# Kernel tuning notes

Hardware: AMD Instinct MI355X
Metric: run time of the kernel (lower is better)

## Reference

```python
import jax, jax.numpy as jnp
import numpy as np

N, E, IN, H, C = 50000, 800000, 128, 256, 2
EPS = 1e-5


def setup_inputs() -> dict:
    key = jax.random.key(0)
    ks = jax.random.split(key, 12)
    inp = {
        "x": jax.random.normal(ks[0], (N, IN), jnp.float32),
        "edge_index": jax.random.randint(ks[1], (2, E), 0, N, jnp.int32),
        "w_nei0": jax.random.normal(ks[2], (IN, H), jnp.float32) * 0.05,
        "w_root0": jax.random.normal(ks[3], (IN, H), jnp.float32) * 0.05,
        "b0": jnp.zeros((H,), jnp.float32),
        "w_nei": jax.random.normal(ks[4], (2, H, H), jnp.float32) * 0.05,
        "w_root": jax.random.normal(ks[5], (2, H, H), jnp.float32) * 0.05,
        "b": jnp.zeros((2, H), jnp.float32),
        "bn_gamma": jnp.ones((3, H), jnp.float32),
        "bn_beta": jnp.zeros((3, H), jnp.float32),
        "bn_mean": jax.random.normal(ks[6], (3, H), jnp.float32) * 0.05,
        "bn_var": jnp.ones((3, H), jnp.float32),
        "w1": jax.random.normal(ks[7], (H, H // 2), jnp.float32) * 0.05,
        "b1": jnp.zeros((H // 2,), jnp.float32),
        "w2": jax.random.normal(ks[8], (H // 2, C), jnp.float32) * 0.05,
        "b2": jnp.zeros((C,), jnp.float32),
    }
    return inp


def _mean_aggregate(h, src, dst, inv_deg):
    # gather source-node features, scatter-sum to destinations, divide by degree
    agg = jax.ops.segment_sum(h[src], dst, num_segments=N)  # (N, d)
    return agg * inv_deg[:, None]


def _forward(x, edge_index, w_nei0, w_root0, b0, w_nei, w_root, b,
             bn_gamma, bn_beta, bn_mean, bn_var, w1, b1, w2, b2):
    src, dst = edge_index[0], edge_index[1]
    deg = jax.ops.segment_sum(jnp.ones((E,), x.dtype), dst, num_segments=N)
    inv_deg = 1.0 / jnp.maximum(deg, 1.0)

    h = x
    wn_list = [w_nei0, w_nei[0], w_nei[1]]
    wr_list = [w_root0, w_root[0], w_root[1]]
    bias_list = [b0, b[0], b[1]]
    for i in range(3):
        mean_nb = _mean_aggregate(h, src, dst, inv_deg)          # (N, d_in)
        h = mean_nb @ wn_list[i] + bias_list[i] + h @ wr_list[i]  # SAGEConv
        # BatchNorm1d (eval: running stats) + ReLU; dropout is identity in eval
        h = (h - bn_mean[i]) * jax.lax.rsqrt(bn_var[i] + EPS) * bn_gamma[i] + bn_beta[i]
        h = jax.nn.relu(h)

    h = jax.nn.relu(h @ w1 + b1)
    logits = h @ w2 + b2
    return jax.nn.log_softmax(logits, axis=1)


def reference(x, edge_index, w_nei0, w_root0, b0, w_nei, w_root, b,
              bn_gamma, bn_beta, bn_mean, bn_var, w1, b1, w2, b2):
    return _forward(x, edge_index, w_nei0, w_root0, b0, w_nei, w_root, b,
                    bn_gamma, bn_beta, bn_mean, bn_var, w1, b1, w2, b2)
```

## Files before the change

### kernel.cpp

```cpp
#include <hip/hip_runtime.h>
#include <hip/hip_fp16.h>

#define N_NODES 50000
#define N_EDGES 800000
#define DIM_IN 128
#define DIM_H 256

typedef _Float16 f16;
typedef _Float16 half8 __attribute__((ext_vector_type(8)));
typedef _Float16 f16x4 __attribute__((ext_vector_type(4)));
typedef _Float16 f16x2 __attribute__((ext_vector_type(2)));
typedef float f32x4 __attribute__((ext_vector_type(4)));
typedef unsigned int u32;
typedef unsigned long long u64;

__device__ __forceinline__ void gload_lds16(const void* g, void* l) {
    __builtin_amdgcn_global_load_lds(
        (const __attribute__((address_space(1))) u32*)g,
        (__attribute__((address_space(3))) u32*)l,
        16, 0, 0);
}


__global__ void k_deg(const int* __restrict__ dst, int* __restrict__ deg) {
    int i = blockIdx.x * 256 + threadIdx.x;
    if (i < N_EDGES) atomicAdd(&deg[dst[i]], 1);
}

__global__ void k_scan1(const int* __restrict__ deg, int* __restrict__ row_start,
                        int* __restrict__ partials) {
    __shared__ int sm[256];
    int t = threadIdx.x;
    int i = blockIdx.x * 256 + t;
    int v = (i < N_NODES) ? deg[i] : 0;
    sm[t] = v;
    __syncthreads();
    for (int ofs = 1; ofs < 256; ofs <<= 1) {
        int add = (t >= ofs) ? sm[t - ofs] : 0;
        __syncthreads();
        sm[t] += add;
        __syncthreads();
    }
    if (i < N_NODES) row_start[i] = sm[t] - v;
    if (t == 255) partials[blockIdx.x] = sm[255];
}

__global__ void k_scan2(const int* __restrict__ partials, int* __restrict__ pscan, int nblk) {
    __shared__ int sm[256];
    int t = threadIdx.x;
    int v = (t < nblk) ? partials[t] : 0;
    sm[t] = v;
    __syncthreads();
    for (int ofs = 1; ofs < 256; ofs <<= 1) {
        int add = (t >= ofs) ? sm[t - ofs] : 0;
        __syncthreads();
        sm[t] += add;
        __syncthreads();
    }
    pscan[t] = sm[t] - v;
}

__global__ void k_scan3(const int* __restrict__ deg, int* __restrict__ row_start,
                        const int* __restrict__ pscan, float* __restrict__ inv_deg) {
    int i = blockIdx.x * 256 + threadIdx.x;
    if (i < N_NODES) {
        row_start[i] += pscan[blockIdx.x];
        int d = deg[i];
        inv_deg[i] = 1.0f / (float)(d > 1 ? d : 1);
        if (i == 0) row_start[N_NODES] = N_EDGES;
    }
}

__global__ void k_fill(const int* __restrict__ src, const int* __restrict__ dst,
                       const int* __restrict__ row_start, int* __restrict__ cursor,
                       int* __restrict__ csr) {
    int i = blockIdx.x * 256 + threadIdx.x;
    if (i < N_EDGES) {
        int d = dst[i];
        int p = atomicAdd(&cursor[d], 1);
        csr[row_start[d] + p] = src[i];
    }
}


__global__ void k_prep(const float* __restrict__ x, f16* __restrict__ hA,
                       const float* __restrict__ wn0, f16* __restrict__ Wn0t,
                       const float* __restrict__ wr0, f16* __restrict__ Wr0t,
                       const float* __restrict__ wn12, f16* __restrict__ Wn1t,
                       f16* __restrict__ Wn2t,
                       const float* __restrict__ wr12, f16* __restrict__ Wr1t,
                       f16* __restrict__ Wr2t,
                       const float* __restrict__ w1, f16* __restrict__ W1t,
                       const float* __restrict__ b0, const float* __restrict__ bvec,
                       const float* __restrict__ gamma, const float* __restrict__ beta,
                       const float* __restrict__ mean, const float* __restrict__ var,
                       const float* __restrict__ b1, float* __restrict__ st,
                       int* __restrict__ deg, int* __restrict__ cursor) {
    const int t = threadIdx.x;
    int b = blockIdx.x;
    auto tcvt = [&](const float* W, f16* Wt, int K, int NN, int bb) {
        int tt = bb * 256 + t;
        int n = tt / K, k = tt - n * K;
        Wt[tt] = (f16)W[(size_t)k * NN + n];
    };
    if (b < 391) {
        int i = b * 256 + t;
        if (i < N_NODES) deg[i] = 0;
        else if (i < 2 * N_NODES) cursor[i - N_NODES] = 0;
    } else if (b < 6641) {
        int i = (b - 391) * 256 + t;
        float4 v = ((const float4*)x)[i];
        f16x4 h = {(f16)v.x, (f16)v.y, (f16)v.z, (f16)v.w};
        *(f16x4*)(hA + (size_t)i * 4) = h;
    } else if (b < 6769) {
        tcvt(wn0, Wn0t, 128, 256, b - 6641);
    } else if (b < 6897) {
        tcvt(wr0, Wr0t, 128, 256, b - 6769);
    } else if (b < 7153) {
        tcvt(wn12, Wn1t, 256, 256, b - 6897);
    } else if (b < 7409) {
        tcvt(wn12 + 65536, Wn2t, 256, 256, b - 7153);
    } else if (b < 7665) {
        tcvt(wr12, Wr1t, 256, 256, b - 7409);
    } else if (b < 7921) {
        tcvt(wr12 + 65536, Wr2t, 256, 256, b - 7665);
    } else if (b < 8049) {
        tcvt(w1, W1t, 256, 128, b - 7921);
    } else {
        int c = t;
        for (int layer = 0; layer < 3; layer++) {
            float bias = (layer == 0) ? b0[c] : bvec[(layer - 1) * DIM_H + c];
            float g = gamma[layer * DIM_H + c];
            float be = beta[layer * DIM_H + c];
            float mu = mean[layer * DIM_H + c];
            float va = var[layer * DIM_H + c];
            float s = g * rsqrtf(va + 1e-5f);
            st[layer * 512 + c] = s;
            st[layer * 512 + 256 + c] = (bias - mu) * s + be;
        }
        st[3 * 512 + c] = 1.0f;
        st[3 * 512 + 256 + c] = (c < 128) ? b1[c] : 0.0f;
    }
}


template <int D>
__global__ void k_agg(const f16* __restrict__ h, const int* __restrict__ row_start,
                      const int* __restrict__ csr, const float* __restrict__ inv_deg,
                      f16* __restrict__ agg) {
    constexpr int V = D / 64;
    typedef _Float16 fvec __attribute__((ext_vector_type(V)));
    int wid = threadIdx.x >> 6;
    int lane = threadIdx.x & 63;
    int v = blockIdx.x * 4 + wid;
    if (v >= N_NODES) return;
    int e0 = row_start[v], e1 = row_start[v + 1];
    float acc[V];
#pragma unroll
    for (int j = 0; j < V; j++) acc[j] = 0.0f;

    const int li = lane & 15;
    for (int e = e0; e < e1; e += 16) {
        int ee = e + li;
        int idx = __builtin_nontemporal_load(&csr[ee < e1 ? ee : e1 - 1]);
        int rem = e1 - e;
        fvec hv[16];
#pragma unroll
        for (int j = 0; j < 16; j++) {
            int s = __shfl(idx, j);
            hv[j] = *(const fvec*)(h + (size_t)s * D + lane * V);
        }
#pragma unroll
        for (int j = 0; j < 16; j++) {
            if (j < rem) {
#pragma unroll
                for (int q = 0; q < V; q++) acc[q] += (float)hv[j][q];
            }
        }
    }

    float sc = inv_deg[v];
    fvec o;
#pragma unroll
    for (int j = 0; j < V; j++) o[j] = (f16)(acc[j] * sc);
    if constexpr (V == 2) {
        u32 raw; __builtin_memcpy(&raw, &o, 4);
        __builtin_nontemporal_store(raw, (u32*)(agg + (size_t)v * D + lane * V));
    } else {
        u64 raw; __builtin_memcpy(&raw, &o, 8);
        __builtin_nontemporal_store(raw, (u64*)(agg + (size_t)v * D + lane * V));
    }
}


__global__ __launch_bounds__(256) void k_gemm(
    const f16* __restrict__ A1, int lda1, const f16* __restrict__ B1, int k1,
    const f16* __restrict__ A2, int lda2, const f16* __restrict__ B2, int k2,
    const float* __restrict__ sc, const float* __restrict__ sh,
    f16* __restrict__ out, int ldo, int M) {
    __shared__ f16 aT[2][64 * 32];
    __shared__ f16 bT[2][256 * 32];
    const int tid = threadIdx.x;
    const int lane = tid & 63;
    const int wid = tid >> 6;
    const int m0 = blockIdx.x * 64;
    f32x4 acc[4][4] = {};

    const int srow = tid >> 2;
    const int schunk = (tid & 3) ^ ((tid >> 3) & 3);
    const int ktot = k1 + k2;

    auto stage = [&](int buf, int kk) {
        const f16 *Ap, *Bp;
        int lda, ldb, kloc;
        if (kk < k1) { Ap = A1; Bp = B1; lda = lda1; ldb = k1; kloc = kk; }
        else         { Ap = A2; Bp = B2; lda = lda2; ldb = k2; kloc = kk - k1; }
        int gm = m0 + srow;
        gm = gm < M ? gm : M - 1;
        gload_lds16(Ap + (size_t)gm * lda + kloc + schunk * 8,
                    (char*)&aT[buf][0] + tid * 16);
#pragma unroll
        for (int hh = 0; hh < 4; hh++) {
            gload_lds16(Bp + (size_t)(hh * 64 + srow) * ldb + kloc + schunk * 8,
                        (char*)&bT[buf][0] + hh * 4096 + tid * 16);
        }
    };

    auto compute = [&](int buf) {
        half8 af[4], bf[4];
#pragma unroll
        for (int mi = 0; mi < 4; mi++) {
            int row = mi * 16 + (lane & 15);
            int ch = (lane >> 4) ^ ((row >> 1) & 3);
            af[mi] = *(const half8*)((const char*)&aT[buf][0] + row * 64 + ch * 16);
        }
#pragma unroll
        for (int ni = 0; ni < 4; ni++) {
            int row = wid * 64 + ni * 16 + (lane & 15);
            int ch = (lane >> 4) ^ ((row >> 1) & 3);
            bf[ni] = *(const half8*)((const char*)&bT[buf][0] + row * 64 + ch * 16);
        }
#pragma unroll
        for (int mi = 0; mi < 4; mi++)
#pragma unroll
            for (int ni = 0; ni < 4; ni++)
                acc[mi][ni] = __builtin_amdgcn_mfma_f32_16x16x32_f16(af[mi], bf[ni],
                                                                     acc[mi][ni], 0, 0, 0);
    };

    stage(0, 0);
    __syncthreads();
    int cur = 0;
    for (int kk = 32; kk < ktot; kk += 32) {
        stage(cur ^ 1, kk);
        compute(cur);
        __syncthreads();
        cur ^= 1;
    }
    compute(cur);

#pragma unroll
    for (int mi = 0; mi < 4; mi++) {
#pragma unroll
        for (int ni = 0; ni < 4; ni++) {
            int gcol = wid * 64 + ni * 16 + (lane & 15);
            float s = sc[gcol], t = sh[gcol];
#pragma unroll
            for (int r = 0; r < 4; r++) {
                int grow = m0 + mi * 16 + (lane >> 4) * 4 + r;
                if (grow < M) {
                    float val = fmaxf(acc[mi][ni][r] * s + t, 0.0f);
                    out[(size_t)grow * ldo + gcol] = (f16)val;
                }
            }
        }
    }
}


__global__ __launch_bounds__(256) void k_gemm_head(
    const f16* __restrict__ A1, int k1, const f16* __restrict__ B1,
    const float* __restrict__ sh,
    const float* __restrict__ w2, const float* __restrict__ b2,
    float* __restrict__ out, int M) {
    __shared__ f16 aT[2][128 * 32];
    __shared__ f16 bT[2][128 * 32];
    __shared__ float smred[128][2][2];
    const int tid = threadIdx.x;
    const int lane = tid & 63;
    const int wid = tid >> 6;
    const int wm = wid >> 1, wn = wid & 1;
    const int m0 = blockIdx.x * 128;
    f32x4 acc[4][4] = {};

    const int srow = tid >> 2;
    const int schunk = (tid & 3) ^ ((tid >> 3) & 3);

    auto stage = [&](int buf, int kk) {
#pragma unroll
        for (int hh = 0; hh < 2; hh++) {
            int r = hh * 64 + srow;
            int gm = m0 + r;
            gm = gm < M ? gm : M - 1;
            gload_lds16(A1 + (size_t)gm * k1 + kk + schunk * 8,
                        (char*)&aT[buf][0] + hh * 4096 + tid * 16);
            gload_lds16(B1 + (size_t)r * k1 + kk + schunk * 8,
                        (char*)&bT[buf][0] + hh * 4096 + tid * 16);
        }
    };

    auto compute = [&](int buf) {
        half8 af[4], bf[4];
#pragma unroll
        for (int mi = 0; mi < 4; mi++) {
            int row = wm * 64 + mi * 16 + (lane & 15);
            int ch = (lane >> 4) ^ ((row >> 1) & 3);
            af[mi] = *(const half8*)((const char*)&aT[buf][0] + row * 64 + ch * 16);
        }
#pragma unroll
        for (int ni = 0; ni < 4; ni++) {
            int row = wn * 64 + ni * 16 + (lane & 15);
            int ch = (lane >> 4) ^ ((row >> 1) & 3);
            bf[ni] = *(const half8*)((const char*)&bT[buf][0] + row * 64 + ch * 16);
        }
#pragma unroll
        for (int mi = 0; mi < 4; mi++)
#pragma unroll
            for (int ni = 0; ni < 4; ni++)
                acc[mi][ni] = __builtin_amdgcn_mfma_f32_16x16x32_f16(af[mi], bf[ni],
                                                                     acc[mi][ni], 0, 0, 0);
    };

    stage(0, 0);
    __syncthreads();
    int cur = 0;
    for (int kk = 32; kk < k1; kk += 32) {
        stage(cur ^ 1, kk);
        compute(cur);
        __syncthreads();
        cur ^= 1;
    }
    compute(cur);

    float w2c[4][2], shc[4];
#pragma unroll
    for (int ni = 0; ni < 4; ni++) {
        int c = wn * 64 + ni * 16 + (lane & 15);
        w2c[ni][0] = w2[c * 2];
        w2c[ni][1] = w2[c * 2 + 1];
        shc[ni] = sh[c];
    }
#pragma unroll
    for (int mi = 0; mi < 4; mi++) {
#pragma unroll
        for (int r = 0; r < 4; r++) {
            float p0 = 0.0f, p1 = 0.0f;
#pragma unroll
            for (int ni = 0; ni < 4; ni++) {
                float val = fmaxf(acc[mi][ni][r] + shc[ni], 0.0f);
                p0 += val * w2c[ni][0];
                p1 += val * w2c[ni][1];
            }
#pragma unroll
            for (int o = 1; o < 16; o <<= 1) {
                p0 += __shfl_xor(p0, o);
                p1 += __shfl_xor(p1, o);
            }
            if ((lane & 15) == 0) {
                int lrow = wm * 64 + mi * 16 + (lane >> 4) * 4 + r;
                smred[lrow][wn][0] = p0;
                smred[lrow][wn][1] = p1;
            }
        }
    }
    __syncthreads();
    if (tid < 128) {
        int grow = m0 + tid;
        if (grow < M) {
            float l0 = smred[tid][0][0] + smred[tid][1][0] + b2[0];
            float l1 = smred[tid][0][1] + smred[tid][1][1] + b2[1];
            float m = fmaxf(l0, l1);
            float lse = m + logf(expf(l0 - m) + expf(l1 - m));
            out[(size_t)grow * 2] = l0 - lse;
            out[(size_t)grow * 2 + 1] = l1 - lse;
        }
    }
}


extern "C" void kernel_launch(void* const* d_in, const int* in_sizes, int n_in,
                              void* d_out, int out_size, void* d_ws, size_t ws_size,
                              hipStream_t stream) {
    const float* x     = (const float*)d_in[0];
    const int*   ei    = (const int*)d_in[1];
    const float* wn0   = (const float*)d_in[2];
    const float* wr0   = (const float*)d_in[3];
    const float* b0    = (const float*)d_in[4];
    const float* wn12  = (const float*)d_in[5];
    const float* wr12  = (const float*)d_in[6];
    const float* bvec  = (const float*)d_in[7];
    const float* gamma = (const float*)d_in[8];
    const float* beta  = (const float*)d_in[9];
    const float* mean  = (const float*)d_in[10];
    const float* var   = (const float*)d_in[11];
    const float* w1    = (const float*)d_in[12];
    const float* b1    = (const float*)d_in[13];
    const float* w2    = (const float*)d_in[14];
    const float* b2    = (const float*)d_in[15];
    const int* srcv = ei;
    const int* dstv = ei + N_EDGES;

    char* p = (char*)d_ws;
    auto alloc = [&](size_t bytes) {
        char* r = p;
        p += (bytes + 255) & ~(size_t)255;
        return r;
    };
    int*   deg       = (int*)alloc((size_t)N_NODES * 4);
    int*   row_start = (int*)alloc((size_t)(N_NODES + 1) * 4);
    int*   cursor    = (int*)alloc((size_t)N_NODES * 4);
    float* inv_deg   = (float*)alloc((size_t)N_NODES * 4);
    int*   partials  = (int*)alloc(256 * 4);
    int*   pscan     = (int*)alloc(256 * 4);
    int*   csr       = (int*)alloc((size_t)N_EDGES * 4);
    f16*   Wn0t      = (f16*)alloc(128 * 256 * 2);
    f16*   Wr0t      = (f16*)alloc(128 * 256 * 2);
    f16*   Wn1t      = (f16*)alloc(256 * 256 * 2);
    f16*   Wr1t      = (f16*)alloc(256 * 256 * 2);
    f16*   Wn2t      = (f16*)alloc(256 * 256 * 2);
    f16*   Wr2t      = (f16*)alloc(256 * 256 * 2);
    f16*   W1t       = (f16*)alloc(256 * 128 * 2);
    float* st        = (float*)alloc(4 * 512 * 4);
    f16*   hA        = (f16*)alloc((size_t)N_NODES * 256 * 2);
    f16*   hB        = (f16*)alloc((size_t)N_NODES * 256 * 2);
    f16*   agg       = (f16*)alloc((size_t)N_NODES * 256 * 2);

    const int EB = (N_EDGES + 255) / 256;
    const int NBLK = (N_NODES + 255) / 256;

    k_prep<<<8050, 256, 0, stream>>>(x, hA, wn0, Wn0t, wr0, Wr0t,
                                     wn12, Wn1t, Wn2t, wr12, Wr1t, Wr2t,
                                     w1, W1t, b0, bvec, gamma, beta, mean, var,
                                     b1, st, deg, cursor);
    k_deg<<<EB, 256, 0, stream>>>(dstv, deg);
    k_scan1<<<NBLK, 256, 0, stream>>>(deg, row_start, partials);
    k_scan2<<<1, 256, 0, stream>>>(partials, pscan, NBLK);
    k_scan3<<<NBLK, 256, 0, stream>>>(deg, row_start, pscan, inv_deg);
    k_fill<<<EB, 256, 0, stream>>>(srcv, dstv, row_start, cursor, csr);

    const int AB = (N_NODES + 3) / 4;
    const int GB = (N_NODES + 63) / 64;

    k_agg<128><<<AB, 256, 0, stream>>>(hA, row_start, csr, inv_deg, agg);
    k_gemm<<<GB, 256, 0, stream>>>(agg, 128, Wn0t, 128, hA, 128, Wr0t, 128,
                                   st + 0, st + 256, hB, 256, N_NODES);
    k_agg<256><<<AB, 256, 0, stream>>>(hB, row_start, csr, inv_deg, agg);
    k_gemm<<<GB, 256, 0, stream>>>(agg, 256, Wn1t, 256, hB, 256, Wr1t, 256,
                                   st + 512, st + 768, hA, 256, N_NODES);
    k_agg<256><<<AB, 256, 0, stream>>>(hA, row_start, csr, inv_deg, agg);
    k_gemm<<<GB, 256, 0, stream>>>(agg, 256, Wn2t, 256, hA, 256, Wr2t, 256,
                                   st + 1024, st + 1280, hB, 256, N_NODES);
    k_gemm_head<<<(N_NODES + 127) / 128, 256, 0, stream>>>(
        hB, 256, W1t, st + 1792, w2, b2, (float*)d_out, N_NODES);
}
```

Before: 357.1 us.

## Enlarge GEMM tile to 128 rows, fuse degree count into prep, drop nontemporal hints

The SAGE GEMM now uses 512-thread blocks covering 128 rows with a 2x4 wave grid, so each staged weight tile is reused across twice as many rows and fewer blocks are launched. The degree-counting atomics move into the prep kernel, with zeroing done by hipMemsetAsync, which removes one launch. The aggregation kernel also drops its nontemporal load and store hints in favour of plain accesses. The larger tile raises LDS and register use per block and may reduce occupancy, and the degree atomics now run alongside the conversion work.

```diff
diff --git a/kernel.cpp b/kernel.cpp
--- a/kernel.cpp
+++ b/kernel.cpp
@@ -12,7 +12,6 @@
 typedef _Float16 f16x2 __attribute__((ext_vector_type(2)));
 typedef float f32x4 __attribute__((ext_vector_type(4)));
 typedef unsigned int u32;
-typedef unsigned long long u64;
 
 __device__ __forceinline__ void gload_lds16(const void* g, void* l) {
     __builtin_amdgcn_global_load_lds(
@@ -21,11 +20,6 @@
         16, 0, 0);
 }
 
-
-__global__ void k_deg(const int* __restrict__ dst, int* __restrict__ deg) {
-    int i = blockIdx.x * 256 + threadIdx.x;
-    if (i < N_EDGES) atomicAdd(&deg[dst[i]], 1);
-}
 
 __global__ void k_scan1(const int* __restrict__ deg, int* __restrict__ row_start,
                         int* __restrict__ partials) {
@@ -95,7 +89,7 @@
                        const float* __restrict__ gamma, const float* __restrict__ beta,
                        const float* __restrict__ mean, const float* __restrict__ var,
                        const float* __restrict__ b1, float* __restrict__ st,
-                       int* __restrict__ deg, int* __restrict__ cursor) {
+                       const int* __restrict__ dst, int* __restrict__ deg) {
     const int t = threadIdx.x;
     int b = blockIdx.x;
     auto tcvt = [&](const float* W, f16* Wt, int K, int NN, int bb) {
@@ -103,30 +97,26 @@
         int n = tt / K, k = tt - n * K;
         Wt[tt] = (f16)W[(size_t)k * NN + n];
     };
-    if (b < 391) {
+    if (b < 6250) {
         int i = b * 256 + t;
-        if (i < N_NODES) deg[i] = 0;
-        else if (i < 2 * N_NODES) cursor[i - N_NODES] = 0;
-    } else if (b < 6641) {
-        int i = (b - 391) * 256 + t;
         float4 v = ((const float4*)x)[i];
         f16x4 h = {(f16)v.x, (f16)v.y, (f16)v.z, (f16)v.w};
         *(f16x4*)(hA + (size_t)i * 4) = h;
-    } else if (b < 6769) {
-        tcvt(wn0, Wn0t, 128, 256, b - 6641);
-    } else if (b < 6897) {
-        tcvt(wr0, Wr0t, 128, 256, b - 6769);
-    } else if (b < 7153) {
-        tcvt(wn12, Wn1t, 256, 256, b - 6897);
-    } else if (b < 7409) {
-        tcvt(wn12 + 65536, Wn2t, 256, 256, b - 7153);
-    } else if (b < 7665) {
-        tcvt(wr12, Wr1t, 256, 256, b - 7409);
-    } else if (b < 7921) {
-        tcvt(wr12 + 65536, Wr2t, 256, 256, b - 7665);
-    } else if (b < 8049) {
-        tcvt(w1, W1t, 256, 128, b - 7921);
-    } else {
+    } else if (b < 6378) {
+        tcvt(wn0, Wn0t, 128, 256, b - 6250);
+    } else if (b < 6506) {
+        tcvt(wr0, Wr0t, 128, 256, b - 6378);
+    } else if (b < 6762) {
+        tcvt(wn12, Wn1t, 256, 256, b - 6506);
+    } else if (b < 7018) {
+        tcvt(wn12 + 65536, Wn2t, 256, 256, b - 6762);
+    } else if (b < 7274) {
+        tcvt(wr12, Wr1t, 256, 256, b - 7018);
+    } else if (b < 7530) {
+        tcvt(wr12 + 65536, Wr2t, 256, 256, b - 7274);
+    } else if (b < 7658) {
+        tcvt(w1, W1t, 256, 128, b - 7530);
+    } else if (b == 7658) {
         int c = t;
         for (int layer = 0; layer < 3; layer++) {
             float bias = (layer == 0) ? b0[c] : bvec[(layer - 1) * DIM_H + c];
@@ -140,6 +130,9 @@
         }
         st[3 * 512 + c] = 1.0f;
         st[3 * 512 + 256 + c] = (c < 128) ? b1[c] : 0.0f;
+    } else {
+        int i = (b - 7659) * 256 + t;
+        if (i < N_EDGES) atomicAdd(&deg[dst[i]], 1);
     }
 }
 
@@ -162,7 +155,7 @@
     const int li = lane & 15;
     for (int e = e0; e < e1; e += 16) {
         int ee = e + li;
-        int idx = __builtin_nontemporal_load(&csr[ee < e1 ? ee : e1 - 1]);
+        int idx = csr[ee < e1 ? ee : e1 - 1];
         int rem = e1 - e;
         fvec hv[16];
 #pragma unroll
@@ -183,27 +176,23 @@
     fvec o;
 #pragma unroll
     for (int j = 0; j < V; j++) o[j] = (f16)(acc[j] * sc);
-    if constexpr (V == 2) {
-        u32 raw; __builtin_memcpy(&raw, &o, 4);
-        __builtin_nontemporal_store(raw, (u32*)(agg + (size_t)v * D + lane * V));
-    } else {
-        u64 raw; __builtin_memcpy(&raw, &o, 8);
-        __builtin_nontemporal_store(raw, (u64*)(agg + (size_t)v * D + lane * V));
-    }
-}
-
-
-__global__ __launch_bounds__(256) void k_gemm(
+    *(fvec*)(agg + (size_t)v * D + lane * V) = o;
+}
+
+
+__global__ __launch_bounds__(512) void k_gemm(
     const f16* __restrict__ A1, int lda1, const f16* __restrict__ B1, int k1,
     const f16* __restrict__ A2, int lda2, const f16* __restrict__ B2, int k2,
     const float* __restrict__ sc, const float* __restrict__ sh,
     f16* __restrict__ out, int ldo, int M) {
-    __shared__ f16 aT[2][64 * 32];
+    __shared__ f16 aT[2][128 * 32];
     __shared__ f16 bT[2][256 * 32];
     const int tid = threadIdx.x;
     const int lane = tid & 63;
     const int wid = tid >> 6;
-    const int m0 = blockIdx.x * 64;
+    const int wm = wid >> 2;
+    const int wn = wid & 3;
+    const int m0 = blockIdx.x * 128;
     f32x4 acc[4][4] = {};
 
     const int srow = tid >> 2;
@@ -220,9 +209,9 @@
         gload_lds16(Ap + (size_t)gm * lda + kloc + schunk * 8,
                     (char*)&aT[buf][0] + tid * 16);
 #pragma unroll
-        for (int hh = 0; hh < 4; hh++) {
-            gload_lds16(Bp + (size_t)(hh * 64 + srow) * ldb + kloc + schunk * 8,
-                        (char*)&bT[buf][0] + hh * 4096 + tid * 16);
+        for (int hh = 0; hh < 2; hh++) {
+            gload_lds16(Bp + (size_t)(hh * 128 + srow) * ldb + kloc + schunk * 8,
+                        (char*)&bT[buf][0] + hh * 8192 + tid * 16);
         }
     };
 
@@ -230,13 +219,13 @@
         half8 af[4], bf[4];
 #pragma unroll
         for (int mi = 0; mi < 4; mi++) {
-            int row = mi * 16 + (lane & 15);
+            int row = wm * 64 + mi * 16 + (lane & 15);
             int ch = (lane >> 4) ^ ((row >> 1) & 3);
             af[mi] = *(const half8*)((const char*)&aT[buf][0] + row * 64 + ch * 16);
         }
 #pragma unroll
         for (int ni = 0; ni < 4; ni++) {
-            int row = wid * 64 + ni * 16 + (lane & 15);
+            int row = wn * 64 + ni * 16 + (lane & 15);
             int ch = (lane >> 4) ^ ((row >> 1) & 3);
             bf[ni] = *(const half8*)((const char*)&bT[buf][0] + row * 64 + ch * 16);
         }
@@ -263,11 +252,11 @@
     for (int mi = 0; mi < 4; mi++) {
 #pragma unroll
         for (int ni = 0; ni < 4; ni++) {
-            int gcol = wid * 64 + ni * 16 + (lane & 15);
+            int gcol = wn * 64 + ni * 16 + (lane & 15);
             float s = sc[gcol], t = sh[gcol];
 #pragma unroll
             for (int r = 0; r < 4; r++) {
-                int grow = m0 + mi * 16 + (lane >> 4) * 4 + r;
+                int grow = m0 + wm * 64 + mi * 16 + (lane >> 4) * 4 + r;
                 if (grow < M) {
                     float val = fmaxf(acc[mi][ni][r] * s + t, 0.0f);
                     out[(size_t)grow * ldo + gcol] = (f16)val;
@@ -435,30 +424,32 @@
     f16*   hB        = (f16*)alloc((size_t)N_NODES * 256 * 2);
     f16*   agg       = (f16*)alloc((size_t)N_NODES * 256 * 2);
 
+    hipMemsetAsync(deg, 0, (size_t)N_NODES * 4, stream);
+    hipMemsetAsync(cursor, 0, (size_t)N_NODES * 4, stream);
+
     const int EB = (N_EDGES + 255) / 256;
     const int NBLK = (N_NODES + 255) / 256;
 
-    k_prep<<<8050, 256, 0, stream>>>(x, hA, wn0, Wn0t, wr0, Wr0t,
-                                     wn12, Wn1t, Wn2t, wr12, Wr1t, Wr2t,
-                                     w1, W1t, b0, bvec, gamma, beta, mean, var,
-                                     b1, st, deg, cursor);
-    k_deg<<<EB, 256, 0, stream>>>(dstv, deg);
+    k_prep<<<10784, 256, 0, stream>>>(x, hA, wn0, Wn0t, wr0, Wr0t,
+                                      wn12, Wn1t, Wn2t, wr12, Wr1t, Wr2t,
+                                      w1, W1t, b0, bvec, gamma, beta, mean, var,
+                                      b1, st, dstv, deg);
     k_scan1<<<NBLK, 256, 0, stream>>>(deg, row_start, partials);
     k_scan2<<<1, 256, 0, stream>>>(partials, pscan, NBLK);
     k_scan3<<<NBLK, 256, 0, stream>>>(deg, row_start, pscan, inv_deg);
     k_fill<<<EB, 256, 0, stream>>>(srcv, dstv, row_start, cursor, csr);
 
     const int AB = (N_NODES + 3) / 4;
-    const int GB = (N_NODES + 63) / 64;
+    const int GB = (N_NODES + 127) / 128;
 
     k_agg<128><<<AB, 256, 0, stream>>>(hA, row_start, csr, inv_deg, agg);
-    k_gemm<<<GB, 256, 0, stream>>>(agg, 128, Wn0t, 128, hA, 128, Wr0t, 128,
+    k_gemm<<<GB, 512, 0, stream>>>(agg, 128, Wn0t, 128, hA, 128, Wr0t, 128,
                                    st + 0, st + 256, hB, 256, N_NODES);
     k_agg<256><<<AB, 256, 0, stream>>>(hB, row_start, csr, inv_deg, agg);
-    k_gemm<<<GB, 256, 0, stream>>>(agg, 256, Wn1t, 256, hB, 256, Wr1t, 256,
+    k_gemm<<<GB, 512, 0, stream>>>(agg, 256, Wn1t, 256, hB, 256, Wr1t, 256,
                                    st + 512, st + 768, hA, 256, N_NODES);
     k_agg<256><<<AB, 256, 0, stream>>>(hA, row_start, csr, inv_deg, agg);
-    k_gemm<<<GB, 256, 0, stream>>>(agg, 256, Wn2t, 256, hA, 256, Wr2t, 256,
+    k_gemm<<<GB, 512, 0, stream>>>(agg, 256, Wn2t, 256, hA, 256, Wr2t, 256,
                                    st + 1024, st + 1280, hB, 256, N_NODES);
     k_gemm_head<<<(N_NODES + 127) / 128, 256, 0, stream>>>(
         hB, 256, W1t, st + 1792, w2, b2, (float*)d_out, N_NODES);
```

Result: faster. 334.7 us (-6.3%).
